# Performance work log

Measured on AMD Instinct MI355X. Metric: run time of the kernel, lower is better.

Reference implementation:

```python
import jax, jax.numpy as jnp
import numpy as np

R_SPHERE = 1.0   # conf['object_bounding_sphere']
N_STEPS = 64     # conf['n_steps']
N_IMPORT = 32    # forward default num_samples
VARI = 0.3       # forward default vari -> inv_s = exp(3)


def sdf_fn(pts):
    # analytic stand-in for implicit_network(x, expression)[..., 0]: sphere of radius 0.5
    return jnp.linalg.norm(pts, axis=-1) - 0.5


def sample_pdf(bins, weights, n_samples):
    # deterministic (det=True) CDF inversion, faithful to sample_pdf()
    weights = weights + 1e-8
    pdf = weights / jnp.sum(weights, -1, keepdims=True)
    cdf = jnp.cumsum(pdf, -1)
    cdf = jnp.concatenate([jnp.zeros_like(cdf[..., :1]), cdf], -1)  # [R, n]
    u = jnp.linspace(0.5 / n_samples, 1.0 - 0.5 / n_samples, n_samples, dtype=bins.dtype)
    u = jnp.broadcast_to(u, cdf.shape[:-1] + (n_samples,))          # [R, ns]
    inds = jax.vmap(lambda c, uu: jnp.searchsorted(c, uu, side='right'))(cdf, u)
    below = jnp.maximum(inds - 1, 0)
    above = jnp.minimum(inds, cdf.shape[-1] - 1)
    cdf_b = jnp.take_along_axis(cdf, below, -1)
    cdf_a = jnp.take_along_axis(cdf, above, -1)
    bins_b = jnp.take_along_axis(bins, below, -1)
    bins_a = jnp.take_along_axis(bins, above, -1)
    denom = cdf_a - cdf_b
    denom = jnp.where(denom < 1e-8, jnp.ones_like(denom), denom)
    t = (u - cdf_b) / denom
    return bins_b + t * (bins_a - bins_b)


def setup_inputs() -> dict:
    key = jax.random.key(0)
    k1, k2 = jax.random.split(key)
    rd = jax.random.normal(k1, (1, 262144, 3), dtype=jnp.float32)
    rd = rd / jnp.linalg.norm(rd, axis=-1, keepdims=True)  # unit ray directions
    cam_loc = jnp.array([[0.0, 0.0, 2.5]], dtype=jnp.float32)  # outside bounding sphere
    t_rand = jax.random.uniform(k2, (262144, N_STEPS), dtype=jnp.float32)
    return {"ray_dirs": rd, "cam_loc": cam_loc, "t_rand": t_rand}


def reference(ray_dirs, cam_loc, t_rand):
    b, p, _ = ray_dirs.shape
    # --- get_sphere_intersection ---
    ray_cam_dot = jnp.einsum('bpd,bd->bp', ray_dirs, cam_loc)              # [b,p]
    under = ray_cam_dot ** 2 - (jnp.sum(cam_loc ** 2, -1, keepdims=True) - R_SPHERE ** 2)
    under = under.reshape(-1)
    mask = under > 0
    sq = jnp.sqrt(jnp.where(mask, under, 0.0))
    si = sq[:, None] * jnp.array([-1.0, 1.0], dtype=ray_dirs.dtype) - ray_cam_dot.reshape(-1)[:, None]
    n_hit = jnp.maximum(jnp.sum(mask), 1)
    mean_si = jnp.sum(jnp.where(mask[:, None], si, 0.0), 0) / n_hit
    si = jnp.where(mask[:, None], si, mean_si[None, :])
    si = jnp.clip(si, 0.0, None)                                           # [b*p, 2]
    min_d, max_d = si[:, 0], si[:, 1]
    # --- eval_sdf_inside_sphere: stratified uniform samples (mask_intersect == all ones) ---
    steps = jnp.linspace(0.0, 1.0, N_STEPS, dtype=ray_dirs.dtype)[None, :]
    steps = steps * (max_d - min_d)[:, None] + min_d[:, None]
    sample_dist = ((max_d - min_d) / N_STEPS)[:, None]
    steps = steps + (t_rand - 0.5) * sample_dist                           # [R, n]
    origins = jnp.broadcast_to(cam_loc[:, None, :], (b, p, 3)).reshape(-1, 3)
    dirs = ray_dirs.reshape(-1, 3)
    pts = origins[:, None, :] + steps[..., None] * dirs[:, None, :]        # [R, n, 3]
    sdf = sdf_fn(pts)                                                      # [R, n]
    # --- NeuS alpha / weights ---
    inv_s = jnp.exp(jnp.asarray(VARI, ray_dirs.dtype) * 10.0)
    prev_cdf = jax.nn.sigmoid(sdf[:, :-1] * inv_s)
    next_cdf = jax.nn.sigmoid(sdf[:, 1:] * inv_s)
    alpha = jnp.clip((prev_cdf - next_cdf + 1e-8) / (prev_cdf + 1e-8), 0.0, 1.0)
    trans = jnp.cumprod(jnp.concatenate([jnp.ones((alpha.shape[0], 1), alpha.dtype),
                                         1.0 - alpha + 1e-7], -1), -1)[:, :-1]
    weights = alpha * trans                                                # [R, n-1]
    # --- up_sample: PDF importance resampling (searchsorted + gather) ---
    z_samples = sample_pdf(steps, weights, N_IMPORT)                       # [R, ns]
    new_samples = origins[:, None, :] + z_samples[..., None] * dirs[:, None, :]  # [R, ns, 3]
    return new_samples, z_samples, weights
```

## Files before the change

kernel.cpp:

```cpp
#include <hip/hip_runtime.h>
#include <hip/hip_bf16.h>


static constexpr int NSTEPS = 64;

__global__ void ws_init_kernel(float* ws){
  int t = blockIdx.x * blockDim.x + threadIdx.x;
  if (t < 3) ws[t] = 0.0f;
}

__global__ __launch_bounds__(256) void si_reduce_kernel(
    const float* __restrict__ rd,
    const float* __restrict__ cam,
    float* __restrict__ ws, int P)
{
  int p = blockIdx.x * blockDim.x + threadIdx.x;
  float cx = cam[0], cy = cam[1], cz = cam[2];
  float c2m = cx*cx + cy*cy + cz*cz - 1.0f;
  float s0 = 0.f, s1 = 0.f, cnt = 0.f;
  if (p < P){
    float dx = rd[3*p+0], dy = rd[3*p+1], dz = rd[3*p+2];
    float rcd = dx*cx + dy*cy + dz*cz;
    float under = rcd*rcd - c2m;
    if (under > 0.f){
      float sq = sqrtf(under);
      s0 = -sq - rcd; s1 = sq - rcd; cnt = 1.f;
    }
  }
  #pragma unroll
  for (int off = 32; off > 0; off >>= 1){
    s0  += __shfl_down(s0,  off, 64);
    s1  += __shfl_down(s1,  off, 64);
    cnt += __shfl_down(cnt, off, 64);
  }
  __shared__ float sh0[4], sh1[4], sh2[4];
  int w = threadIdx.x >> 6, lane = threadIdx.x & 63;
  if (lane == 0){ sh0[w] = s0; sh1[w] = s1; sh2[w] = cnt; }
  __syncthreads();
  if (threadIdx.x == 0){
    atomicAdd(&ws[0], sh0[0]+sh0[1]+sh0[2]+sh0[3]);
    atomicAdd(&ws[1], sh1[0]+sh1[1]+sh1[2]+sh1[3]);
    atomicAdd(&ws[2], sh2[0]+sh2[1]+sh2[2]+sh2[3]);
  }
}

__global__ __launch_bounds__(256) void render_main_kernel(
    const float* __restrict__ rd,
    const float* __restrict__ cam,
    const float* __restrict__ tr,
    const float* __restrict__ ws,
    float* __restrict__ out, int P)
{
  const int lane = threadIdx.x & 63;
  const int p = blockIdx.x * (blockDim.x >> 6) + (threadIdx.x >> 6);
  if (p >= P) return;

  float cx = cam[0], cy = cam[1], cz = cam[2];
  float c2m = cx*cx + cy*cy + cz*cz - 1.0f;
  float dx = rd[3*p+0], dy = rd[3*p+1], dz = rd[3*p+2];
  float rcd = dx*cx + dy*cy + dz*cz;
  float under = rcd*rcd - c2m;
  float si0, si1;
  if (under > 0.f){
    float sq = sqrtf(under);
    si0 = -sq - rcd; si1 = sq - rcd;
  } else {
    float nh = fmaxf(ws[2], 1.0f);
    si0 = ws[0] / nh; si1 = ws[1] / nh;
  }
  float min_d = fmaxf(si0, 0.f), max_d = fmaxf(si1, 0.f);
  float range = max_d - min_d;
  float sdist = range * (1.0f / NSTEPS);

  float trand = tr[(size_t)p * NSTEPS + lane];
  float stepv = min_d + range * ((float)lane * (1.0f/63.0f)) + (trand - 0.5f) * sdist;

  float px = cx + stepv*dx, py = cy + stepv*dy, pz = cz + stepv*dz;
  float sdf = sqrtf(px*px + py*py + pz*pz) - 0.5f;
  const float inv_s = 20.085536923187668f;
  float c = 1.0f / (1.0f + __expf(-sdf * inv_s));

  float cnext = __shfl_down(c, 1, 64);
  float alpha = 0.f;
  if (lane < 63){
    alpha = (c - cnext + 1e-8f) / (c + 1e-8f);
    alpha = fminf(fmaxf(alpha, 0.f), 1.0f);
  }

  float f = 1.0f - alpha + 1e-7f;
  float prod = f;
  #pragma unroll
  for (int off = 1; off < 64; off <<= 1){
    float o = __shfl_up(prod, off, 64);
    if (lane >= off) prod *= o;
  }
  float trans = __shfl_up(prod, 1, 64);
  if (lane == 0) trans = 1.0f;
  float wgt = alpha * trans;

  float wp = (lane < 63) ? (wgt + 1e-8f) : 0.f;
  float s = wp;
  #pragma unroll
  for (int off = 1; off < 64; off <<= 1){
    float o = __shfl_up(s, off, 64);
    if (lane >= off) s += o;
  }
  float T  = __shfl(s, 63, 64);
  float ex = __shfl_up(s, 1, 64);
  if (lane == 0) ex = 0.f;
  float cdf = ex / T;

  int i = lane & 31;
  float u = (float)(2*i + 1) * (1.0f / 64.0f);
  int pos = 0;
  #pragma unroll
  for (int st = 32; st > 0; st >>= 1){
    int idx = pos + st - 1; idx = idx > 63 ? 63 : idx;
    float cv = __shfl(cdf, idx, 64);
    if (cv <= u) pos += st;
  }
  int below = pos - 1; if (below < 0) below = 0;
  int above = pos < 63 ? pos : 63;
  float cdf_b = __shfl(cdf,  below, 64);
  float cdf_a = __shfl(cdf,  above, 64);
  float bin_b = __shfl(stepv, below, 64);
  float bin_a = __shfl(stepv, above, 64);
  float denom = cdf_a - cdf_b;
  if (denom < 1e-8f) denom = 1.0f;
  float t = (u - cdf_b) / denom;
  float z = bin_b + t * (bin_a - bin_b);

  const size_t P96  = (size_t)P * 96;
  const size_t P128 = (size_t)P * 128;
  if (lane < 32){
    float nx = cx + z*dx, ny = cy + z*dy, nz = cz + z*dz;
    size_t base = (size_t)p * 96 + (size_t)lane * 3;
    out[base + 0] = nx;
    out[base + 1] = ny;
    out[base + 2] = nz;
    out[P96 + (size_t)p * 32 + lane] = z;
  }
  if (lane < 63){
    out[P128 + (size_t)p * 63 + lane] = wgt;
  }
}

extern "C" void kernel_launch(void* const* d_in, const int* in_sizes, int n_in,
                              void* d_out, int out_size, void* d_ws, size_t ws_size,
                              hipStream_t stream) {
  const float* rd  = (const float*)d_in[0];
  const float* cam = (const float*)d_in[1];
  const float* tr  = (const float*)d_in[2];
  float* out = (float*)d_out;
  float* ws  = (float*)d_ws;
  const int P = in_sizes[0] / 3;

  ws_init_kernel<<<1, 64, 0, stream>>>(ws);
  si_reduce_kernel<<<(P + 255) / 256, 256, 0, stream>>>(rd, cam, ws, P);
  const int raysPerBlock = 4;
  render_main_kernel<<<(P + raysPerBlock - 1) / raysPerBlock, 256, 0, stream>>>(
      rd, cam, tr, ws, out, P);
}
```

Baseline: 366.7 us.

## Process one ray per thread with serial scans and merged CDF sampling

The main kernel now gives each ray to one thread instead of one 64-lane wavefront. The transmittance cumprod and CDF are computed with serial loops, and importance samples are produced by a single merged walk over the CDF rather than shuffle-based scans and a binary search. Inputs are read as float4. The sphere-intersection mean reduction replaces the init kernel and global atomics with a grid-stride partial-sum kernel plus a one-block final kernel. This removes the many cross-lane shuffles, but per-thread strided stores and higher register pressure from the per-thread arrays may hurt memory coalescing and occupancy.

New measurement: 410.6 us. 1.12x slower.

```diff
diff --git a/kernel.cpp b/kernel.cpp
--- a/kernel.cpp
+++ b/kernel.cpp
@@ -1,30 +1,24 @@
 #include <hip/hip_runtime.h>
-#include <hip/hip_bf16.h>
 
 
 static constexpr int NSTEPS = 64;
+static constexpr int NIMP   = 32;
 
-__global__ void ws_init_kernel(float* ws){
-  int t = blockIdx.x * blockDim.x + threadIdx.x;
-  if (t < 3) ws[t] = 0.0f;
-}
-
-__global__ __launch_bounds__(256) void si_reduce_kernel(
-    const float* __restrict__ rd,
-    const float* __restrict__ cam,
-    float* __restrict__ ws, int P)
+__global__ __launch_bounds__(256) void si_partial_kernel(
+    const float* __restrict__ rd, const float* __restrict__ cam,
+    float* __restrict__ partial, int P)
 {
-  int p = blockIdx.x * blockDim.x + threadIdx.x;
   float cx = cam[0], cy = cam[1], cz = cam[2];
   float c2m = cx*cx + cy*cy + cz*cz - 1.0f;
   float s0 = 0.f, s1 = 0.f, cnt = 0.f;
-  if (p < P){
+  int stride = gridDim.x * blockDim.x;
+  for (int p = blockIdx.x * blockDim.x + threadIdx.x; p < P; p += stride){
     float dx = rd[3*p+0], dy = rd[3*p+1], dz = rd[3*p+2];
     float rcd = dx*cx + dy*cy + dz*cz;
     float under = rcd*rcd - c2m;
     if (under > 0.f){
       float sq = sqrtf(under);
-      s0 = -sq - rcd; s1 = sq - rcd; cnt = 1.f;
+      s0 += -sq - rcd; s1 += sq - rcd; cnt += 1.f;
     }
   }
   #pragma unroll
@@ -33,26 +27,47 @@
     s1  += __shfl_down(s1,  off, 64);
     cnt += __shfl_down(cnt, off, 64);
   }
-  __shared__ float sh0[4], sh1[4], sh2[4];
-  int w = threadIdx.x >> 6, lane = threadIdx.x & 63;
-  if (lane == 0){ sh0[w] = s0; sh1[w] = s1; sh2[w] = cnt; }
+  __shared__ float sh[3][4];
+  int w = threadIdx.x >> 6;
+  if ((threadIdx.x & 63) == 0){ sh[0][w] = s0; sh[1][w] = s1; sh[2][w] = cnt; }
   __syncthreads();
   if (threadIdx.x == 0){
-    atomicAdd(&ws[0], sh0[0]+sh0[1]+sh0[2]+sh0[3]);
-    atomicAdd(&ws[1], sh1[0]+sh1[1]+sh1[2]+sh1[3]);
-    atomicAdd(&ws[2], sh2[0]+sh2[1]+sh2[2]+sh2[3]);
+    partial[blockIdx.x*3+0] = sh[0][0]+sh[0][1]+sh[0][2]+sh[0][3];
+    partial[blockIdx.x*3+1] = sh[1][0]+sh[1][1]+sh[1][2]+sh[1][3];
+    partial[blockIdx.x*3+2] = sh[2][0]+sh[2][1]+sh[2][2]+sh[2][3];
+  }
+}
+
+__global__ __launch_bounds__(256) void si_final_kernel(
+    const float* __restrict__ partial, float* __restrict__ ws, int nblk)
+{
+  float s0 = 0.f, s1 = 0.f, cnt = 0.f;
+  for (int b = threadIdx.x; b < nblk; b += 256){
+    s0 += partial[3*b+0]; s1 += partial[3*b+1]; cnt += partial[3*b+2];
+  }
+  #pragma unroll
+  for (int off = 32; off > 0; off >>= 1){
+    s0  += __shfl_down(s0,  off, 64);
+    s1  += __shfl_down(s1,  off, 64);
+    cnt += __shfl_down(cnt, off, 64);
+  }
+  __shared__ float sh[3][4];
+  int w = threadIdx.x >> 6;
+  if ((threadIdx.x & 63) == 0){ sh[0][w] = s0; sh[1][w] = s1; sh[2][w] = cnt; }
+  __syncthreads();
+  if (threadIdx.x == 0){
+    ws[0] = sh[0][0]+sh[0][1]+sh[0][2]+sh[0][3];
+    ws[1] = sh[1][0]+sh[1][1]+sh[1][2]+sh[1][3];
+    ws[2] = sh[2][0]+sh[2][1]+sh[2][2]+sh[2][3];
   }
 }
 
 __global__ __launch_bounds__(256) void render_main_kernel(
-    const float* __restrict__ rd,
-    const float* __restrict__ cam,
-    const float* __restrict__ tr,
-    const float* __restrict__ ws,
+    const float* __restrict__ rd, const float* __restrict__ cam,
+    const float* __restrict__ tr, const float* __restrict__ ws,
     float* __restrict__ out, int P)
 {
-  const int lane = threadIdx.x & 63;
-  const int p = blockIdx.x * (blockDim.x >> 6) + (threadIdx.x >> 6);
+  int p = blockIdx.x * blockDim.x + threadIdx.x;
   if (p >= P) return;
 
   float cx = cam[0], cy = cam[1], cz = cam[2];
@@ -72,76 +87,69 @@
   float range = max_d - min_d;
   float sdist = range * (1.0f / NSTEPS);
 
-  float trand = tr[(size_t)p * NSTEPS + lane];
-  float stepv = min_d + range * ((float)lane * (1.0f/63.0f)) + (trand - 0.5f) * sdist;
-
-  float px = cx + stepv*dx, py = cy + stepv*dy, pz = cz + stepv*dz;
-  float sdf = sqrtf(px*px + py*py + pz*pz) - 0.5f;
-  const float inv_s = 20.085536923187668f;
-  float c = 1.0f / (1.0f + __expf(-sdf * inv_s));
-
-  float cnext = __shfl_down(c, 1, 64);
-  float alpha = 0.f;
-  if (lane < 63){
-    alpha = (c - cnext + 1e-8f) / (c + 1e-8f);
-    alpha = fminf(fmaxf(alpha, 0.f), 1.0f);
+  float steps[NSTEPS];
+  const float4* tr4 = (const float4*)(tr + (size_t)p * NSTEPS);
+  #pragma unroll
+  for (int q = 0; q < 16; q++){
+    float4 v = tr4[q];
+    steps[4*q+0] = fmaf(range, (float)(4*q+0) * (1.0f/63.0f), min_d) + (v.x - 0.5f) * sdist;
+    steps[4*q+1] = fmaf(range, (float)(4*q+1) * (1.0f/63.0f), min_d) + (v.y - 0.5f) * sdist;
+    steps[4*q+2] = fmaf(range, (float)(4*q+2) * (1.0f/63.0f), min_d) + (v.z - 0.5f) * sdist;
+    steps[4*q+3] = fmaf(range, (float)(4*q+3) * (1.0f/63.0f), min_d) + (v.w - 0.5f) * sdist;
   }
 
-  float f = 1.0f - alpha + 1e-7f;
-  float prod = f;
+  const float inv_s = 20.085536923187668f;
+  float w[NSTEPS-1];
+  float T = 0.f, trans = 1.f;
+  float px = fmaf(steps[0], dx, cx), py = fmaf(steps[0], dy, cy), pz = fmaf(steps[0], dz, cz);
+  float c0 = 1.0f / (1.0f + __expf(-(sqrtf(px*px+py*py+pz*pz) - 0.5f) * inv_s));
   #pragma unroll
-  for (int off = 1; off < 64; off <<= 1){
-    float o = __shfl_up(prod, off, 64);
-    if (lane >= off) prod *= o;
+  for (int j = 0; j < NSTEPS-1; j++){
+    float qx = fmaf(steps[j+1], dx, cx), qy = fmaf(steps[j+1], dy, cy), qz = fmaf(steps[j+1], dz, cz);
+    float c1 = 1.0f / (1.0f + __expf(-(sqrtf(qx*qx+qy*qy+qz*qz) - 0.5f) * inv_s));
+    float a = (c0 - c1 + 1e-8f) / (c0 + 1e-8f);
+    a = fminf(fmaxf(a, 0.f), 1.0f);
+    float wj = a * trans;
+    w[j] = wj;
+    T += wj;
+    trans *= (1.0f - a + 1e-7f);
+    c0 = c1;
   }
-  float trans = __shfl_up(prod, 1, 64);
-  if (lane == 0) trans = 1.0f;
-  float wgt = alpha * trans;
+  T += 63.0f * 1e-8f;
+  float invT = 1.0f / T;
 
-  float wp = (lane < 63) ? (wgt + 1e-8f) : 0.f;
-  float s = wp;
+  float* wout = out + (size_t)P*128 + (size_t)p*63;
   #pragma unroll
-  for (int off = 1; off < 64; off <<= 1){
-    float o = __shfl_up(s, off, 64);
-    if (lane >= off) s += o;
+  for (int j = 0; j < NSTEPS-1; j++) wout[j] = w[j];
+
+  float* zout = out + (size_t)P*96 + (size_t)p*32;
+  float* nout = out + (size_t)p*96;
+  int i = 0;
+  float cdf_m = 0.f;
+  #pragma unroll
+  for (int m = 0; m < NSTEPS-1; m++){
+    float cdf_n = cdf_m + (w[m] + 1e-8f) * invT;
+    while (i < NIMP){
+      float u = (float)(2*i + 1) * (1.0f / 64.0f);
+      if (!(u < cdf_n)) break;
+      float denom = cdf_n - cdf_m;
+      if (denom < 1e-8f) denom = 1.0f;
+      float t = (u - cdf_m) / denom;
+      float z = fmaf(t, steps[m+1] - steps[m], steps[m]);
+      zout[i] = z;
+      nout[3*i+0] = fmaf(z, dx, cx);
+      nout[3*i+1] = fmaf(z, dy, cy);
+      nout[3*i+2] = fmaf(z, dz, cz);
+      i++;
+    }
+    cdf_m = cdf_n;
   }
-  float T  = __shfl(s, 63, 64);
-  float ex = __shfl_up(s, 1, 64);
-  if (lane == 0) ex = 0.f;
-  float cdf = ex / T;
-
-  int i = lane & 31;
-  float u = (float)(2*i + 1) * (1.0f / 64.0f);
-  int pos = 0;
-  #pragma unroll
-  for (int st = 32; st > 0; st >>= 1){
-    int idx = pos + st - 1; idx = idx > 63 ? 63 : idx;
-    float cv = __shfl(cdf, idx, 64);
-    if (cv <= u) pos += st;
-  }
-  int below = pos - 1; if (below < 0) below = 0;
-  int above = pos < 63 ? pos : 63;
-  float cdf_b = __shfl(cdf,  below, 64);
-  float cdf_a = __shfl(cdf,  above, 64);
-  float bin_b = __shfl(stepv, below, 64);
-  float bin_a = __shfl(stepv, above, 64);
-  float denom = cdf_a - cdf_b;
-  if (denom < 1e-8f) denom = 1.0f;
-  float t = (u - cdf_b) / denom;
-  float z = bin_b + t * (bin_a - bin_b);
-
-  const size_t P96  = (size_t)P * 96;
-  const size_t P128 = (size_t)P * 128;
-  if (lane < 32){
-    float nx = cx + z*dx, ny = cy + z*dy, nz = cz + z*dz;
-    size_t base = (size_t)p * 96 + (size_t)lane * 3;
-    out[base + 0] = nx;
-    out[base + 1] = ny;
-    out[base + 2] = nz;
-    out[P96 + (size_t)p * 32 + lane] = z;
-  }
-  if (lane < 63){
-    out[P128 + (size_t)p * 63 + lane] = wgt;
+  float zl = steps[NSTEPS-1];
+  float nx = fmaf(zl, dx, cx), ny = fmaf(zl, dy, cy), nz = fmaf(zl, dz, cz);
+  while (i < NIMP){
+    zout[i] = zl;
+    nout[3*i+0] = nx; nout[3*i+1] = ny; nout[3*i+2] = nz;
+    i++;
   }
 }
 
@@ -155,9 +163,8 @@
   float* ws  = (float*)d_ws;
   const int P = in_sizes[0] / 3;
 
-  ws_init_kernel<<<1, 64, 0, stream>>>(ws);
-  si_reduce_kernel<<<(P + 255) / 256, 256, 0, stream>>>(rd, cam, ws, P);
-  const int raysPerBlock = 4;
-  render_main_kernel<<<(P + raysPerBlock - 1) / raysPerBlock, 256, 0, stream>>>(
-      rd, cam, tr, ws, out, P);
+  const int RBLK = 256;
+  si_partial_kernel<<<RBLK, 256, 0, stream>>>(rd, cam, ws + 8, P);
+  si_final_kernel<<<1, 256, 0, stream>>>(ws + 8, ws, RBLK);
+  render_main_kernel<<<(P + 255) / 256, 256, 0, stream>>>(rd, cam, tr, ws, out, P);
 }
```
